# Kernel tuning notes

Measured on AMD Instinct MI355X. Metric: run time of the kernel, lower is better.

Reference implementation:

```python
import jax, jax.numpy as jnp
import numpy as np

B, S, D, HEADS, E, HID = 4, 2048, 512, 8, 8, 1365  # HID = int(D*4*2/3) per Expert_alt
CF, THRESH, TOPN = 2.0, 0.2, 2                      # capacity_factor_eval, threshold_eval, top-2
BAL_COEF, Z_COEF = 0.01, 0.001


def setup_inputs():
    key = jax.random.key(0)
    ks = jax.random.split(key, 8)
    f32 = jnp.float32
    return {
        'x': jax.random.normal(ks[0], (B, S, D), f32),
        'Wqkv': jax.random.normal(ks[1], (3 * D, D), f32) * (D ** -0.5),
        'bqkv': jnp.zeros((3 * D,), f32),
        'Wo': jax.random.normal(ks[2], (D, D), f32) * (D ** -0.5),
        'bo': jnp.zeros((D,), f32),
        'Wg': jax.random.normal(ks[3], (D, E), f32) * (D ** -0.5),
        'ln_g': jnp.ones((E, D), f32),
        'ln_b': jnp.zeros((E, D), f32),
        'W1': jax.random.normal(ks[4], (E, D, HID), f32) * (D ** -0.5),
        'b1': jnp.zeros((E, HID), f32),
        'W2': jax.random.normal(ks[5], (E, HID, D), f32) * (HID ** -0.5),
        'b2': jnp.zeros((E, D), f32),
    }


def _moe(x, Wg, ln_g, ln_b, W1, b1, W2, b2):
    # top-2 gated MoE with capacity-factor dispatch, grouped expert FFN, combine
    Bq, Sq, Dq = x.shape
    Eq = Wg.shape[1]
    C = int(CF * Sq * TOPN / Eq)  # expert capacity per batch row
    logits = x @ Wg                              # [B,S,E]
    probs = jax.nn.softmax(logits, -1)
    gvals, gidx = jax.lax.top_k(probs, 2)        # [B,S,2]
    use2 = (gvals[..., 1] > THRESH).astype(x.dtype)
    # priority order: all top-1 assignments first, then top-2
    e_idx = jnp.concatenate([gidx[..., 0], gidx[..., 1]], axis=1)          # [B,2S]
    assigned = jnp.concatenate([jnp.ones((Bq, Sq), x.dtype), use2], axis=1)
    onehot = jax.nn.one_hot(e_idx, Eq, dtype=x.dtype) * assigned[..., None]
    pos = (jnp.cumsum(onehot, axis=1) * onehot).sum(-1) - 1.0              # slot within expert
    keep = ((assigned > 0) & (pos >= 0) & (pos < C)).astype(x.dtype)
    slot = jnp.where(keep > 0, pos, C).astype(jnp.int32)                   # overflow -> slot C (dropped)
    b_idx = jnp.broadcast_to(jnp.arange(Bq)[:, None], (Bq, 2 * Sq))
    x2 = jnp.concatenate([x, x], axis=1) * keep[..., None]
    disp = jnp.zeros((Bq, Eq, C + 1, Dq), x.dtype).at[b_idx, e_idx, slot].add(x2)
    # grouped expert FFN: LayerNorm -> Linear -> LeakyReLU -> Linear
    xe = disp[:, :, :C].transpose(1, 0, 2, 3).reshape(Eq, Bq * C, Dq)
    mu = xe.mean(-1, keepdims=True)
    var = xe.var(-1, keepdims=True)
    xn = (xe - mu) * jax.lax.rsqrt(var + 1e-5) * ln_g[:, None] + ln_b[:, None]
    h = jnp.einsum('etd,edh->eth', xn, W1) + b1[:, None]
    h = jnp.where(h > 0, h, 0.01 * h)  # LeakyReLU
    ye = jnp.einsum('eth,ehd->etd', h, W2) + b2[:, None]
    yb = ye.reshape(Eq, Bq, C, Dq).transpose(1, 0, 2, 3)                   # [B,E,C,D]
    yb = jnp.concatenate([yb, jnp.zeros((Bq, Eq, 1, Dq), x.dtype)], axis=2)
    y_tok = yb[b_idx, e_idx, slot]                                         # [B,2S,D]
    w = jnp.concatenate([gvals[..., 0], gvals[..., 1] * use2], axis=1) * keep
    out = (y_tok * w[..., None]).reshape(Bq, 2, Sq, Dq).sum(1)
    # aux losses
    top1 = jax.nn.one_hot(gidx[..., 0], Eq, dtype=x.dtype)
    density = top1.mean((0, 1))
    proxy = probs.mean((0, 1))
    balance = Eq * jnp.sum(density * proxy)
    zloss = jnp.mean(jax.nn.logsumexp(logits, -1) ** 2)
    total = BAL_COEF * balance + Z_COEF * zloss
    return out, total, balance, zloss


def reference(x, Wqkv, bqkv, Wo, bo, Wg, ln_g, ln_b, W1, b1, W2, b2):
    Bq, Sq, Dq = x.shape
    dh = Dq // HEADS
    qkv = x @ Wqkv.T + bqkv
    q, k, v = jnp.split(qkv, 3, -1)
    rs = lambda t: t.reshape(Bq, Sq, HEADS, dh).transpose(0, 2, 1, 3)
    q, k, v = rs(q), rs(k), rs(v)
    attn = jax.nn.softmax(jnp.einsum('bhqd,bhkd->bhqk', q, k) / np.float32(np.sqrt(dh)), -1)
    o = jnp.einsum('bhqk,bhkd->bhqd', attn, v).transpose(0, 2, 1, 3).reshape(Bq, Sq, Dq)
    o = o @ Wo.T + bo + x  # MHA + residual
    moe_out, total, bal, z = _moe(o, Wg, ln_g, ln_b, W1, b1, W2, b2)
    return moe_out + o, total, bal, z  # SparseMoEBlock residual; dropout is identity (eval)
```

## Files before the change

kernel.cpp:

```cpp
#include <hip/hip_runtime.h>
#include <hip/hip_bf16.h>
#include <math.h>

#define B_    4
#define S_    2048
#define D_    512
#define H_    8
#define DH_   64
#define E_    8
#define HID_  1365
#define HIDP_ 1408
#define CAP_  1024
#define TOK_  (B_*S_)
#define NASS_ (B_*2*S_)
#define RMAX_ (NASS_ + 8*128)

typedef __attribute__((ext_vector_type(8))) short bf16x8;
typedef __attribute__((ext_vector_type(4))) float f32x4;
typedef __hip_bfloat16 bf16;

#define MFMA16(a, b, c) __builtin_amdgcn_mfma_f32_16x16x32_bf16(a, b, c, 0, 0, 0)

__device__ __forceinline__ void gload16(const void* g, void* l) {
  __builtin_amdgcn_global_load_lds(
      (const __attribute__((address_space(1))) unsigned int*)g,
      (__attribute__((address_space(3))) unsigned int*)l, 16, 0, 0);
}

__device__ __forceinline__ unsigned bf16pk(float a, float b) {
  unsigned ua = __float_as_uint(a); ua = (ua + 0x7FFF + ((ua >> 16) & 1)) >> 16;
  unsigned ub = __float_as_uint(b); ub = (ub + 0x7FFF + ((ub >> 16) & 1)) >> 16;
  return ua | (ub << 16);
}

__device__ __forceinline__ unsigned short bf16rne(float x, float& back) {
  unsigned u = __float_as_uint(x);
  unsigned r = (u + 0x7FFF + ((u >> 16) & 1)) >> 16;
  back = __uint_as_float(r << 16);
  return (unsigned short)r;
}

__global__ __launch_bounds__(256) void cvt_bf16(const float* __restrict__ in,
                                                bf16* __restrict__ out, int n) {
  int i = (blockIdx.x * 256 + threadIdx.x) * 4;
  if (i < n) {
    float4 v = *(const float4*)(in + i);
    uint2 pk; pk.x = bf16pk(v.x, v.y); pk.y = bf16pk(v.z, v.w);
    *(uint2*)((unsigned short*)out + i) = pk;
  }
}

__global__ __launch_bounds__(256) void split3v(const float* __restrict__ in,
    unsigned short* __restrict__ ph, unsigned short* __restrict__ pm,
    unsigned short* __restrict__ pl, int n) {
  int i = (blockIdx.x * 256 + threadIdx.x) * 4;
  if (i >= n) return;
  float4 v = *(const float4*)(in + i);
  float a[4] = {v.x, v.y, v.z, v.w};
  ushort4 hh, mm, ll;
  unsigned short* hp = (unsigned short*)&hh;
  unsigned short* mp = (unsigned short*)&mm;
  unsigned short* lp = (unsigned short*)&ll;
#pragma unroll
  for (int j = 0; j < 4; j++) {
    float fh, fm, fl;
    hp[j] = bf16rne(a[j], fh);
    float r = a[j] - fh;
    mp[j] = bf16rne(r, fm);
    float r2 = r - fm;
    lp[j] = bf16rne(r2, fl);
  }
  *(ushort4*)(ph + i) = hh;
  *(ushort4*)(pm + i) = mm;
  *(ushort4*)(pl + i) = ll;
}

__global__ __launch_bounds__(256) void transpose_w1(const float* __restrict__ W1,
                                                    bf16* __restrict__ W1t) {
  __shared__ float t[32][33];
  int e = blockIdx.z;
  int n0 = blockIdx.x * 32, d0 = blockIdx.y * 32;
  int tx = threadIdx.x & 31, ty = threadIdx.x >> 5;
  const float* in = W1 + (size_t)e * D_ * HID_;
  bf16* out = W1t + (size_t)e * HIDP_ * D_;
#pragma unroll
  for (int j = 0; j < 4; j++) {
    int d = d0 + ty + j * 8, n = n0 + tx;
    t[ty + j * 8][tx] = (n < HID_) ? in[(size_t)d * HID_ + n] : 0.f;
  }
  __syncthreads();
#pragma unroll
  for (int j = 0; j < 4; j++) {
    int n = n0 + ty + j * 8, d = d0 + tx;
    out[(size_t)n * D_ + d] = __float2bfloat16(t[tx][ty + j * 8]);
  }
}

__global__ __launch_bounds__(256) void transpose_w2(const float* __restrict__ W2,
                                                    bf16* __restrict__ W2t) {
  __shared__ float t[32][33];
  int e = blockIdx.z;
  int n0 = blockIdx.x * 32, k0 = blockIdx.y * 32;
  int tx = threadIdx.x & 31, ty = threadIdx.x >> 5;
  const float* in = W2 + (size_t)e * HID_ * D_;
  bf16* out = W2t + (size_t)e * D_ * HIDP_;
#pragma unroll
  for (int j = 0; j < 4; j++) {
    int k = k0 + ty + j * 8;
    t[ty + j * 8][tx] = (k < HID_) ? in[(size_t)k * D_ + n0 + tx] : 0.f;
  }
  __syncthreads();
#pragma unroll
  for (int j = 0; j < 4; j++) {
    int n = n0 + ty + j * 8, k = k0 + tx;
    out[(size_t)n * HIDP_ + k] = __float2bfloat16(t[tx][ty + j * 8]);
  }
}

__global__ __launch_bounds__(256) void transpose_v(const bf16* __restrict__ vbuf,
                                                   bf16* __restrict__ vT) {
  __shared__ bf16 t[32][33];
  int bh = blockIdx.z;
  int b = bh >> 3, h = bh & 7;
  int s0 = blockIdx.x * 32, d0 = blockIdx.y * 32;
  int tx = threadIdx.x & 31, ty = threadIdx.x >> 5;
  const bf16* in = vbuf + (size_t)b * S_ * D_ + h * DH_;
#pragma unroll
  for (int j = 0; j < 4; j++)
    t[ty + j * 8][tx] = in[(size_t)(s0 + ty + j * 8) * D_ + d0 + tx];
  __syncthreads();
  bf16* out = vT + (size_t)bh * DH_ * S_;
#pragma unroll
  for (int j = 0; j < 4; j++)
    out[(size_t)(d0 + ty + j * 8) * S_ + s0 + tx] = t[tx][ty + j * 8];
}

__global__ __launch_bounds__(256) void transpose_u(const float* __restrict__ U32,
                                                   bf16* __restrict__ U2T) {
  __shared__ float t[64][132];
  int b = blockIdx.y;
  int s0 = blockIdx.x * 64;
  int tid = threadIdx.x;
#pragma unroll
  for (int p = 0; p < 8; p++) {
    int i = tid + p * 256;
    int tok = i >> 5, c4 = i & 31;
    float4 v = *(const float4*)(U32 + (size_t)(b * 2048 + s0 + tok) * 128 + c4 * 4);
    t[tok][c4 * 4 + 0] = v.x; t[tok][c4 * 4 + 1] = v.y;
    t[tok][c4 * 4 + 2] = v.z; t[tok][c4 * 4 + 3] = v.w;
  }
  __syncthreads();
  int row = tid >> 1, sh = tid & 1;
  int h = row >> 4, rr = row & 15;
  int e = rr & 7;
  bool lo = rr >= 8;
  bf16* dst = U2T + ((size_t)((b * 8 + h) * 16 + rr) * 2048 + s0 + sh * 32);
  for (int i = 0; i < 32; i++) {
    float v = t[sh * 32 + i][h * 8 + e];
    float back;
    unsigned short hh = bf16rne(v, back);
    unsigned short outv;
    if (lo) { float b2; outv = bf16rne(v - back, b2); }
    else outv = hh;
    ((unsigned short*)dst)[i] = outv;
  }
}

template <int MODE>
__global__ __launch_bounds__(256) void gemm_mfma(
    const bf16* __restrict__ A, const bf16* __restrict__ Bt,
    const float* __restrict__ bias, const float* __restrict__ resid,
    void* __restrict__ Cout, int N, int K,
    const int* __restrict__ ebase, const int* __restrict__ ecnt) {
  __shared__ bf16 Al[128 * 64];
  __shared__ bf16 Bl[128 * 64];
  int tid = threadIdx.x;
  int w = tid >> 6, lane = tid & 63;
  int lg = lane >> 4, li = lane & 15;
  int e = 0;
  size_t arow0;
  if constexpr (MODE >= 2) {
    e = blockIdx.z;
    int r0 = blockIdx.y * 128;
    if (r0 >= ecnt[e]) return;
    arow0 = (size_t)(ebase[e] + r0);
  } else {
    arow0 = (size_t)blockIdx.y * 128;
  }
  int n0 = blockIdx.x * 128;
  const bf16* Bexp = Bt + (size_t)e * N * K;

  int rowA[4], scA[4];
#pragma unroll
  for (int j = 0; j < 4; j++) {
    int o = w * 4096 + j * 1024 + lane * 16;
    rowA[j] = o >> 7;
    scA[j] = ((o >> 4) & 7) ^ (rowA[j] & 7);
  }
  int wm = w >> 1, wn = w & 1;
  f32x4 acc[4][4] = {};

  for (int k0 = 0; k0 < K; k0 += 64) {
#pragma unroll
    for (int j = 0; j < 4; j++) {
      int o = w * 4096 + j * 1024 + lane * 16;
      gload16(A + (arow0 + rowA[j]) * (size_t)K + k0 + scA[j] * 8, (char*)Al + o);
      gload16(Bexp + (size_t)(n0 + rowA[j]) * K + k0 + scA[j] * 8, (char*)Bl + o);
    }
    __syncthreads();
#pragma unroll
    for (int ks = 0; ks < 2; ks++) {
      bf16x8 af[4], bfr[4];
#pragma unroll
      for (int mi = 0; mi < 4; mi++) {
        int row = wm * 64 + mi * 16 + li;
        int cb = (lg * 16 + ks * 64) ^ ((row & 7) << 4);
        af[mi] = *(const bf16x8*)((char*)Al + row * 128 + cb);
      }
#pragma unroll
      for (int ni = 0; ni < 4; ni++) {
        int row = wn * 64 + ni * 16 + li;
        int cb = (lg * 16 + ks * 64) ^ ((row & 7) << 4);
        bfr[ni] = *(const bf16x8*)((char*)Bl + row * 128 + cb);
      }
#pragma unroll
      for (int mi = 0; mi < 4; mi++)
#pragma unroll
        for (int ni = 0; ni < 4; ni++)
          acc[mi][ni] = MFMA16(af[mi], bfr[ni], acc[mi][ni]);
    }
    __syncthreads();
  }

#pragma unroll
  for (int mi = 0; mi < 4; mi++) {
#pragma unroll
    for (int ni = 0; ni < 4; ni++) {
#pragma unroll
      for (int r = 0; r < 4; r++) {
        size_t m = arow0 + wm * 64 + mi * 16 + lg * 4 + r;
        int c = n0 + wn * 64 + ni * 16 + li;
        float v = acc[mi][ni][r];
        if constexpr (MODE == 0) {
          v += bias[c];
          ((bf16*)Cout)[m * (size_t)N + c] = __float2bfloat16(v);
        } else if constexpr (MODE == 1) {
          v += bias[c] + resid[m * (size_t)N + c];
          ((float*)Cout)[m * (size_t)N + c] = v;
        } else if constexpr (MODE == 2) {
          if (c < HID_) {
            v += bias[e * HID_ + c];
            v = (v > 0.f) ? v : 0.01f * v;
            ((bf16*)Cout)[m * (size_t)HIDP_ + c] = __float2bfloat16(v);
          } else {
            ((bf16*)Cout)[m * (size_t)HIDP_ + c] = __float2bfloat16(0.f);
          }
        } else {
          v += bias[e * D_ + c];
          ((bf16*)Cout)[m * (size_t)N + c] = __float2bfloat16(v);
        }
      }
    }
  }
}

__global__ __launch_bounds__(256) void gemm_split3(
    const bf16* __restrict__ Ah, const bf16* __restrict__ Am, const bf16* __restrict__ Al_,
    const bf16* __restrict__ Bh, const bf16* __restrict__ Bm, const bf16* __restrict__ Bl_,
    const float* __restrict__ bias, float* __restrict__ C, int N, int K) {
  __shared__ bf16 Ls[6][128 * 32];
  const bf16* Ap[3] = {Ah, Am, Al_};
  const bf16* Bp[3] = {Bh, Bm, Bl_};
  int tid = threadIdx.x;
  int w = tid >> 6, lane = tid & 63;
  int lg = lane >> 4, li = lane & 15;
  int lin = blockIdx.y * gridDim.x + blockIdx.x;
  int lxn = (gridDim.x == 8) ? 3 : 0;
  int ytile = (lin & 7) + ((lin >> (3 + lxn)) << 3);
  int xtile = (lin >> 3) & (gridDim.x - 1);
  size_t m0 = (size_t)ytile * 128;
  int n0 = xtile * 128;
  int wm = w >> 1, wn = w & 1;
  f32x4 acc[4][4] = {};

  for (int k0 = 0; k0 < K; k0 += 32) {
#pragma unroll
    for (int p = 0; p < 3; p++) {
#pragma unroll
      for (int j = 0; j < 2; j++) {
        int o = w * 2048 + j * 1024 + lane * 16;
        int row = o >> 6;
        int sc = ((o >> 4) & 3) ^ (row & 3);
        gload16(Ap[p] + (m0 + row) * (size_t)K + k0 + sc * 8, (char*)Ls[p] + o);
        gload16(Bp[p] + (size_t)(n0 + row) * K + k0 + sc * 8, (char*)Ls[3 + p] + o);
      }
    }
    __syncthreads();
    bf16x8 af[3][4], bfv[3][4];
#pragma unroll
    for (int p = 0; p < 3; p++) {
#pragma unroll
      for (int mi = 0; mi < 4; mi++) {
        int row = wm * 64 + mi * 16 + li;
        int cb = (lg * 16) ^ ((row & 3) << 4);
        af[p][mi] = *(const bf16x8*)((char*)Ls[p] + row * 64 + cb);
      }
#pragma unroll
      for (int ni = 0; ni < 4; ni++) {
        int row = wn * 64 + ni * 16 + li;
        int cb = (lg * 16) ^ ((row & 3) << 4);
        bfv[p][ni] = *(const bf16x8*)((char*)Ls[3 + p] + row * 64 + cb);
      }
    }
#pragma unroll
    for (int mi = 0; mi < 4; mi++)
#pragma unroll
      for (int ni = 0; ni < 4; ni++) {
        acc[mi][ni] = MFMA16(af[0][mi], bfv[0][ni], acc[mi][ni]);
        acc[mi][ni] = MFMA16(af[0][mi], bfv[1][ni], acc[mi][ni]);
        acc[mi][ni] = MFMA16(af[1][mi], bfv[0][ni], acc[mi][ni]);
        acc[mi][ni] = MFMA16(af[1][mi], bfv[1][ni], acc[mi][ni]);
        acc[mi][ni] = MFMA16(af[0][mi], bfv[2][ni], acc[mi][ni]);
        acc[mi][ni] = MFMA16(af[2][mi], bfv[0][ni], acc[mi][ni]);
      }
    __syncthreads();
  }
#pragma unroll
  for (int mi = 0; mi < 4; mi++)
#pragma unroll
    for (int ni = 0; ni < 4; ni++)
#pragma unroll
      for (int r = 0; r < 4; r++) {
        size_t m = m0 + wm * 64 + mi * 16 + lg * 4 + r;
        int c = n0 + wn * 64 + ni * 16 + li;
        C[m * (size_t)N + c] = acc[mi][ni][r] + bias[c];
      }
}

__global__ __launch_bounds__(256) void ksplit(const float* __restrict__ qk32,
    unsigned short* __restrict__ kh, unsigned short* __restrict__ km,
    unsigned short* __restrict__ kl) {
  int gid = blockIdx.x * 256 + threadIdx.x;
  int idx4 = gid * 4;
  int t = idx4 >> 9, c = idx4 & 511;
  int h = c >> 6, d = c & 63;
  int b = t >> 11, s = t & 2047;
  float4 v = *(const float4*)(qk32 + (size_t)t * 1024 + 512 + c);
  float a[4] = {v.x, v.y, v.z, v.w};
  ushort4 hh, mm, ll;
  unsigned short* hp = (unsigned short*)&hh;
  unsigned short* mp = (unsigned short*)&mm;
  unsigned short* lp = (unsigned short*)&ll;
#pragma unroll
  for (int j = 0; j < 4; j++) {
    float fh, fm, fl;
    hp[j] = bf16rne(a[j], fh);
    float r = a[j] - fh;
    mp[j] = bf16rne(r, fm);
    float r2 = r - fm;
    lp[j] = bf16rne(r2, fl);
  }
  size_t o = (((size_t)(b * 8 + h) * S_ + s) * 64 + d);
  *(ushort4*)(kh + o) = hh;
  *(ushort4*)(km + o) = mm;
  *(ushort4*)(kl + o) = ll;
}

__global__ __launch_bounds__(256) void wg2_kernel(const float* __restrict__ Wo,
                                                  const float* __restrict__ Wg,
                                                  float* __restrict__ Wg2) {
  int gid = blockIdx.x * 256 + threadIdx.x;
  int d = gid >> 3, e = gid & 7;
  float acc = 0.f;
  for (int n = 0; n < D_; n++) acc += Wo[(size_t)n * D_ + d] * Wg[n * E_ + e];
  Wg2[d * E_ + e] = acc;
}

__global__ __launch_bounds__(256) void wu_kernel(const float* __restrict__ Wqkv,
    const float* __restrict__ Wg2, const float* __restrict__ bqkv,
    float* __restrict__ Wu, float* __restrict__ bU) {
  int gid = blockIdx.x * 256 + threadIdx.x;
  int row = gid >> 9, d = gid & 511;
  float acc = 0.f;
  if (row < 64) {
    int h = row >> 3, e = row & 7;
    const float* wv = Wqkv + (size_t)(1024 + h * 64) * 512 + d;
    const float* wg = Wg2 + h * 64 * 8 + e;
    for (int c = 0; c < 64; c++) acc += wv[(size_t)c * 512] * wg[c * 8];
  }
  Wu[gid] = acc;
  if (gid < 128) {
    float bacc = 0.f;
    if (gid < 64) {
      int h = gid >> 3, e = gid & 7;
      for (int c = 0; c < 64; c++)
        bacc += bqkv[1024 + h * 64 + c] * Wg2[(h * 64 + c) * 8 + e];
    }
    bU[gid] = bacc;
  }
}

__global__ __launch_bounds__(256) void xwg_kernel(const float* __restrict__ x,
                                                  const float* __restrict__ bo,
                                                  const float* __restrict__ Wg,
                                                  float* __restrict__ logits) {
  int tid = threadIdx.x;
  int tl = tid >> 3, j = tid & 7;
  int t = blockIdx.x * 32 + tl;
  const float* xr = x + (size_t)t * D_;
  float part[8] = {0, 0, 0, 0, 0, 0, 0, 0};
  for (int d = j; d < D_; d += 8) {
    float xv = xr[d] + bo[d];
    const float* wg = Wg + d * E_;
#pragma unroll
    for (int e = 0; e < 8; e++) part[e] += xv * wg[e];
  }
#pragma unroll
  for (int off = 1; off < 8; off <<= 1)
#pragma unroll
    for (int e = 0; e < 8; e++) part[e] += __shfl_xor(part[e], off);
  if (j == 0) {
#pragma unroll
    for (int e = 0; e < 8; e++) logits[(size_t)t * 8 + e] = part[e];
  }
}

__global__ __launch_bounds__(512, 4) void attn_fused(
    const float* __restrict__ qk32,
    const bf16* __restrict__ kh, const bf16* __restrict__ km,
    const bf16* __restrict__ kl,
    const bf16* __restrict__ vT, const bf16* __restrict__ U2T,
    bf16* __restrict__ attnb, float* __restrict__ part) {
  __shared__ bf16 Ks0[128 * 64];
  __shared__ bf16 Ks1[128 * 64];
  __shared__ bf16 Ks2[128 * 64];
  __shared__ bf16 Vtl[64 * 128];
  __shared__ bf16 Ut[16 * 128];
  __shared__ bf16 Pl[8][16 * 40];
  int bid = blockIdx.x;
  int xcd = bid & 7, idx = bid >> 3;
  int bh = (idx >> 4) * 8 + xcd;
  int qt = idx & 15;
  int b = bh >> 3, h = bh & 7, q0 = qt * 128;
  int tid = threadIdx.x, w = tid >> 6, lane = tid & 63;
  int lg = lane >> 4, qi = lane & 15;

  const float* qsrc = qk32 + (size_t)(b * S_ + q0 + w * 16 + qi) * 1024 + h * 64 + lg * 8;
  bf16x8 qh[2], qm[2], ql[2];
#pragma unroll
  for (int ks = 0; ks < 2; ks++) {
#pragma unroll
    for (int i = 0; i < 8; i++) {
      float xv = qsrc[ks * 32 + i];
      float fh, fm, fl;
      unsigned short ah = bf16rne(xv, fh);
      float r = xv - fh;
      unsigned short am = bf16rne(r, fm);
      float r2 = r - fm;
      unsigned short al = bf16rne(r2, fl);
      ((unsigned short*)&qh[ks])[i] = ah;
      ((unsigned short*)&qm[ks])[i] = am;
      ((unsigned short*)&ql[ks])[i] = al;
    }
  }

  f32x4 oacc[4] = {};
  f32x4 racc = {0.f, 0.f, 0.f, 0.f};
  float mrun = -1e30f, lrun = 0.f;
  const bf16* Vbase = vT + (size_t)bh * DH_ * S_;
  char* pw = (char*)&Pl[w][0];

  for (int kt = 0; kt < S_ / 128; kt++) {
#pragma unroll
    for (int j = 0; j < 2; j++) {
      int o = w * 2048 + j * 1024 + lane * 16;
      int row = o >> 7;
      int sc = ((o >> 4) & 7) ^ (row & 7);
      size_t srcK = ((size_t)bh * S_ + kt * 128 + row) * 64 + sc * 8;
      gload16(kh + srcK, (char*)Ks0 + o);
      gload16(km + srcK, (char*)Ks1 + o);
      gload16(kl + srcK, (char*)Ks2 + o);
      int rowv = o >> 8;
      int scv = ((o >> 4) & 15) ^ (rowv & 7);
      gload16(Vbase + (size_t)rowv * S_ + kt * 128 + scv * 8, (char*)Vtl + o);
    }
    if (w < 2) {
#pragma unroll
      for (int j = 0; j < 2; j++) {
        int o = w * 2048 + j * 1024 + lane * 16;
        int rowu = o >> 8;
        int scu = ((o >> 4) & 15) ^ (rowu & 7);
        gload16(U2T + ((size_t)(bh * 16 + rowu) * 2048 + kt * 128 + scu * 8),
                (char*)Ut + o);
      }
    }
    __syncthreads();

    f32x4 sacc[8];
#pragma unroll
    for (int nb = 0; nb < 8; nb++) { f32x4 z = {0.f, 0.f, 0.f, 0.f}; sacc[nb] = z; }
#pragma unroll
    for (int ks = 0; ks < 2; ks++) {
#pragma unroll
      for (int nb = 0; nb < 8; nb++) {
        int row = nb * 16 + qi;
        int cb = (lg * 16 + ks * 64) ^ ((row & 7) << 4);
        bf16x8 k0 = *(const bf16x8*)((char*)Ks0 + row * 128 + cb);
        bf16x8 k1 = *(const bf16x8*)((char*)Ks1 + row * 128 + cb);
        bf16x8 k2 = *(const bf16x8*)((char*)Ks2 + row * 128 + cb);
        sacc[nb] = MFMA16(k0, qh[ks], sacc[nb]);
        sacc[nb] = MFMA16(k0, qm[ks], sacc[nb]);
        sacc[nb] = MFMA16(k1, qh[ks], sacc[nb]);
        sacc[nb] = MFMA16(k1, qm[ks], sacc[nb]);
        sacc[nb] = MFMA16(k2, qh[ks], sacc[nb]);
        sacc[nb] = MFMA16(k0, ql[ks], sacc[nb]);
      }
    }
    float tmax = -1e30f;
#pragma unroll
    for (int nb = 0; nb < 8; nb++)
#pragma unroll
      for (int r = 0; r < 4; r++) {
        float v = sacc[nb][r] * 0.125f;
        sacc[nb][r] = v;
        tmax = fmaxf(tmax, v);
      }
    tmax = fmaxf(tmax, __shfl_xor(tmax, 16));
    tmax = fmaxf(tmax, __shfl_xor(tmax, 32));
    float mnew = fmaxf(mrun, tmax);
    float fsc = __expf(mrun - mnew);
    float psum = 0.f;
#pragma unroll
    for (int nb = 0; nb < 8; nb++)
#pragma unroll
      for (int r = 0; r < 4; r++) {
        float pv = __expf(sacc[nb][r] - mnew);
        sacc[nb][r] = pv;
        psum += pv;
      }
    psum += __shfl_xor(psum, 16);
    psum += __shfl_xor(psum, 32);
    lrun = lrun * fsc + psum;
    mrun = mnew;
#pragma unroll
    for (int r = 0; r < 4; r++) racc[r] *= fsc;
#pragma unroll
    for (int db = 0; db < 4; db++)
#pragma unroll
      for (int r = 0; r < 4; r++) oacc[db][r] *= fsc;

#pragma unroll
    for (int c = 0; c < 4; c++) {
#pragma unroll
      for (int nbL = 0; nbL < 2; nbL++) {
        int nb = c * 2 + nbL;
#pragma unroll
        for (int rp = 0; rp < 2; rp++) {
          unsigned pk = bf16pk(sacc[nb][rp * 2], sacc[nb][rp * 2 + 1]);
          int keyl = 4 * lg + 2 * rp + 16 * nbL;
          *(unsigned*)(pw + qi * 80 + keyl * 2) = pk;
        }
      }
      bf16x8 pf = *(const bf16x8*)(pw + qi * 80 + lg * 16);
#pragma unroll
      for (int db = 0; db < 4; db++) {
        int row = db * 16 + qi;
        int cb = (lg * 16 + c * 64) ^ ((row & 7) << 4);
        bf16x8 vf = *(const bf16x8*)((char*)Vtl + row * 256 + cb);
        oacc[db] = MFMA16(vf, pf, oacc[db]);
      }
      int ua = qi * 256 + ((c * 64 + lg * 16) ^ ((qi & 7) << 4));
      bf16x8 uf = *(const bf16x8*)((char*)Ut + ua);
      racc = MFMA16(uf, pf, racc);
#pragma unroll
      for (int nbL = 0; nbL < 2; nbL++) {
        int nb = c * 2 + nbL;
#pragma unroll
        for (int rp = 0; rp < 2; rp++) {
          float p0 = sacc[nb][rp * 2], p1 = sacc[nb][rp * 2 + 1];
          float b0, b1v;
          bf16rne(p0, b0); bf16rne(p1, b1v);
          unsigned pkl = bf16pk(p0 - b0, p1 - b1v);
          int keyl = 4 * lg + 2 * rp + 16 * nbL;
          *(unsigned*)(pw + qi * 80 + keyl * 2) = pkl;
        }
      }
      bf16x8 pfl = *(const bf16x8*)(pw + qi * 80 + lg * 16);
      racc = MFMA16(uf, pfl, racc);
    }
    __syncthreads();
  }

  float inv = 1.f / lrun;
#pragma unroll
  for (int r = 0; r < 4; r++) racc[r] += __shfl_xor(racc[r], 32);
  if (lg < 2) {
    float* dst = part + ((size_t)bh * S_ + q0 + w * 16 + qi) * 8 + lg * 4;
#pragma unroll
    for (int r = 0; r < 4; r++) dst[r] = racc[r] * inv;
  }
  char* ow = (char*)Ks0 + w * 2048;
#pragma unroll
  for (int db = 0; db < 4; db++)
#pragma unroll
    for (int rp = 0; rp < 2; rp++) {
      int d = db * 16 + lg * 4 + rp * 2;
      unsigned pk = bf16pk(oacc[db][rp * 2] * inv, oacc[db][rp * 2 + 1] * inv);
      int addr = (qi * 128 + d * 2) ^ ((qi & 7) << 4);
      *(unsigned*)(ow + addr) = pk;
    }
#pragma unroll
  for (int j = 0; j < 2; j++) {
    int o = j * 1024 + lane * 16;
    int q = o >> 7;
    int c16 = (o >> 4) & 7;
    int sc = c16 ^ (q & 7);
    bf16x8 vv = *(const bf16x8*)(ow + q * 128 + sc * 16);
    *(bf16x8*)(attnb + ((size_t)(b * S_ + q0 + w * 16 + q)) * D_ + h * DH_ + c16 * 8) = vv;
  }
}

__global__ __launch_bounds__(256) void reduce_gate(
    const float* __restrict__ xwg, const float* __restrict__ part,
    int* __restrict__ e1a, int* __restrict__ e2a,
    float* __restrict__ g1a, float* __restrict__ g2a, int* __restrict__ use2a,
    float* __restrict__ dacc) {
  int t = blockIdx.x * 256 + threadIdx.x;
  int b = t >> 11, s = t & 2047;
  float lg[8];
#pragma unroll
  for (int e = 0; e < 8; e++) lg[e] = xwg[(size_t)t * 8 + e];
  for (int h = 0; h < 8; h++) {
    const float* pp = part + ((size_t)(b * 8 + h) * S_ + s) * 8;
#pragma unroll
    for (int e = 0; e < 8; e++) lg[e] += pp[e];
  }
  float mx = lg[0];
#pragma unroll
  for (int e = 1; e < 8; e++) mx = fmaxf(mx, lg[e]);
  float p[8], se = 0.f;
#pragma unroll
  for (int e = 0; e < 8; e++) { p[e] = expf(lg[e] - mx); se += p[e]; }
  float inv = 1.f / se;
#pragma unroll
  for (int e = 0; e < 8; e++) p[e] *= inv;
  float lse = logf(se) + mx;
  int a1 = 0; float m1 = p[0];
#pragma unroll
  for (int e = 1; e < 8; e++) if (p[e] > m1) { m1 = p[e]; a1 = e; }
  int a2 = -1; float m2 = -1.f;
#pragma unroll
  for (int e = 0; e < 8; e++) if (e != a1 && p[e] > m2) { m2 = p[e]; a2 = e; }
  e1a[t] = a1; e2a[t] = a2; g1a[t] = m1; g2a[t] = m2;
  use2a[t] = (m2 > 0.2f) ? 1 : 0;
  float z = lse * lse;
  float pr[8];
#pragma unroll
  for (int e = 0; e < 8; e++) pr[e] = p[e];
#pragma unroll
  for (int off = 1; off < 64; off <<= 1) {
#pragma unroll
    for (int e = 0; e < 8; e++) pr[e] += __shfl_xor(pr[e], off);
    z += __shfl_xor(z, off);
  }
  float dcnt[8];
#pragma unroll
  for (int e = 0; e < 8; e++) dcnt[e] = (float)__popcll(__ballot(a1 == e));
  if ((threadIdx.x & 63) == 0) {
#pragma unroll
    for (int e = 0; e < 8; e++) {
      atomicAdd(&dacc[e], dcnt[e]);
      atomicAdd(&dacc[8 + e], pr[e]);
    }
    atomicAdd(&dacc[16], z);
  }
}

__global__ __launch_bounds__(512) void scan_kernel(
    const int* __restrict__ e1a, const int* __restrict__ e2a,
    const int* __restrict__ use2a,
    int* __restrict__ posArr, int* __restrict__ kept_be) {
  __shared__ int wcnt[8][8];
  int b = blockIdx.x;
  int w = threadIdx.x >> 6, lane = threadIdx.x & 63;
  unsigned long long below = (1ull << lane) - 1ull;
  int cnt[8] = {0, 0, 0, 0, 0, 0, 0, 0};
  int ev[8], av[8];
#pragma unroll
  for (int it = 0; it < 8; it++) {
    int i = w * 512 + it * 64 + lane;
    int s = i & (S_ - 1);
    int t = b * S_ + s;
    int e, a;
    if (i < S_) { e = e1a[t]; a = 1; }
    else        { e = e2a[t]; a = use2a[t]; }
    ev[it] = e; av[it] = a;
#pragma unroll
    for (int ee = 0; ee < 8; ee++)
      cnt[ee] += __popcll(__ballot(a && (e == ee)));
  }
  if (lane == 0)
#pragma unroll
    for (int ee = 0; ee < 8; ee++) wcnt[w][ee] = cnt[ee];
  __syncthreads();
  int run[8];
#pragma unroll
  for (int ee = 0; ee < 8; ee++) {
    int sB = 0;
    for (int ww = 0; ww < w; ww++) sB += wcnt[ww][ee];
    run[ee] = sB;
  }
#pragma unroll
  for (int it = 0; it < 8; it++) {
    int i = w * 512 + it * 64 + lane;
    int e = ev[it], a = av[it];
    int pos = -1;
#pragma unroll
    for (int ee = 0; ee < 8; ee++) {
      unsigned long long mask = __ballot(a && (e == ee));
      if (a && e == ee) pos = run[ee] + __popcll(mask & below);
      run[ee] += __popcll(mask);
    }
    posArr[b * (2 * S_) + i] = (a && pos < CAP_) ? pos : -1;
  }
  if (w == 7 && lane == 0)
#pragma unroll
    for (int ee = 0; ee < 8; ee++) kept_be[b * 8 + ee] = min(run[ee], CAP_);
}

__global__ void finalize_meta(const int* __restrict__ kept_be,
                              int* __restrict__ ebase, int* __restrict__ bbase,
                              int* __restrict__ ecnt,
                              const float* __restrict__ dacc, float* __restrict__ outs) {
  if (threadIdx.x == 0 && blockIdx.x == 0) {
    int base = 0;
    for (int e = 0; e < 8; e++) {
      int tot = 0;
      for (int b = 0; b < 4; b++) { bbase[b * 8 + e] = tot; tot += kept_be[b * 8 + e]; }
      ecnt[e] = tot;
      ebase[e] = base;
      base += (tot + 127) & ~127;
    }
    float bal = 0.f;
    for (int e = 0; e < 8; e++) bal += (dacc[e] / (float)TOK_) * (dacc[8 + e] / (float)TOK_);
    bal *= (float)E_;
    float z = dacc[16] / (float)TOK_;
    outs[0] = 0.01f * bal + 0.001f * z;
    outs[1] = bal;
    outs[2] = z;
  }
}

__global__ __launch_bounds__(256) void scatter_kernel(
    const int* __restrict__ posArr, const int* __restrict__ e1a, const int* __restrict__ e2a,
    const float* __restrict__ g1a, const float* __restrict__ g2a,
    const int* __restrict__ ebase, const int* __restrict__ bbase,
    int* __restrict__ rowtok, int* __restrict__ rowexp,
    int* __restrict__ tokidx, float* __restrict__ tokw) {
  int gi = blockIdx.x * 256 + threadIdx.x;
  int b = gi >> 12, i = gi & 4095;
  int k = i >> 11, s = i & (S_ - 1);
  int t = b * S_ + s;
  int pos = posArr[gi];
  int idx = -1; float w = 0.f;
  if (pos >= 0) {
    int e = k ? e2a[t] : e1a[t];
    idx = ebase[e] + bbase[b * 8 + e] + pos;
    rowtok[idx] = t;
    rowexp[idx] = e;
    w = k ? g2a[t] : g1a[t];
  }
  tokidx[k * TOK_ + t] = idx;
  tokw[k * TOK_ + t] = w;
}

__global__ __launch_bounds__(256) void ln_kernel(
    const float* __restrict__ o2, const int* __restrict__ rowtok,
    const int* __restrict__ rowexp, const float* __restrict__ ln_g,
    const float* __restrict__ ln_b, bf16* __restrict__ xn) {
  int row = blockIdx.x * 4 + (threadIdx.x >> 6);
  int lane = threadIdx.x & 63;
  int tok = rowtok[row];
  if (tok < 0) return;
  int e = rowexp[row];
  const float* xr = o2 + (size_t)tok * D_;
  float v[8], sum = 0.f, sq = 0.f;
#pragma unroll
  for (int j = 0; j < 8; j++) { v[j] = xr[lane * 8 + j]; sum += v[j]; sq += v[j] * v[j]; }
#pragma unroll
  for (int off = 1; off < 64; off <<= 1) { sum += __shfl_xor(sum, off); sq += __shfl_xor(sq, off); }
  float mu = sum / (float)D_;
  float var = sq / (float)D_ - mu * mu;
  float inv = rsqrtf(var + 1e-5f);
  bf16* xo = xn + (size_t)row * D_;
#pragma unroll
  for (int j = 0; j < 8; j++) {
    int d = lane * 8 + j;
    xo[d] = __float2bfloat16((v[j] - mu) * inv * ln_g[e * D_ + d] + ln_b[e * D_ + d]);
  }
}

__global__ __launch_bounds__(256) void combine_kernel(
    const float* __restrict__ o2, const bf16* __restrict__ y,
    const int* __restrict__ tokidx, const float* __restrict__ tokw,
    float* __restrict__ out) {
  size_t gi = (size_t)blockIdx.x * 256 + threadIdx.x;
  int t = (int)(gi >> 9);
  int d = (int)(gi & (D_ - 1));
  float v = o2[gi];
  int i1 = tokidx[t], i2 = tokidx[TOK_ + t];
  if (i1 >= 0) v += tokw[t] * __bfloat162float(y[(size_t)i1 * D_ + d]);
  if (i2 >= 0) v += tokw[TOK_ + t] * __bfloat162float(y[(size_t)i2 * D_ + d]);
  out[gi] = v;
}

extern "C" void kernel_launch(void* const* d_in, const int* in_sizes, int n_in,
                              void* d_out, int out_size, void* d_ws, size_t ws_size,
                              hipStream_t stream) {
  const float* x    = (const float*)d_in[0];
  const float* Wqkv = (const float*)d_in[1];
  const float* bqkv = (const float*)d_in[2];
  const float* Wo   = (const float*)d_in[3];
  const float* bo   = (const float*)d_in[4];
  const float* Wg   = (const float*)d_in[5];
  const float* ln_g = (const float*)d_in[6];
  const float* ln_b = (const float*)d_in[7];
  const float* W1   = (const float*)d_in[8];
  const float* b1   = (const float*)d_in[9];
  const float* W2   = (const float*)d_in[10];
  const float* b2   = (const float*)d_in[11];
  float* out = (float*)d_out;

  char* ws = (char*)d_ws;
  size_t off = 0;
  auto alloc = [&](size_t bytes) -> void* {
    void* p = ws + off;
    off = (off + bytes + 255) & ~(size_t)255;
    return p;
  };
  float* qk32  = (float*)alloc((size_t)TOK_ * 1024 * 4);
  bf16* vbuf   = (bf16*)alloc((size_t)TOK_ * D_ * 2);
  bf16* vT     = (bf16*)alloc((size_t)B_ * H_ * DH_ * S_ * 2);
  bf16* attnb  = (bf16*)alloc((size_t)TOK_ * D_ * 2);
  float* o2    = (float*)alloc((size_t)TOK_ * D_ * 4);
  bf16* xh     = (bf16*)alloc((size_t)TOK_ * D_ * 2);
  bf16* xm     = (bf16*)alloc((size_t)TOK_ * D_ * 2);
  bf16* xl     = (bf16*)alloc((size_t)TOK_ * D_ * 2);
  bf16* Wqh    = (bf16*)alloc((size_t)1024 * D_ * 2);
  bf16* Wqm    = (bf16*)alloc((size_t)1024 * D_ * 2);
  bf16* Wql    = (bf16*)alloc((size_t)1024 * D_ * 2);
  bf16* Wvb    = (bf16*)alloc((size_t)D_ * D_ * 2);
  bf16* Wob    = (bf16*)alloc((size_t)D_ * D_ * 2);
  bf16* W1t    = (bf16*)alloc((size_t)E_ * HIDP_ * D_ * 2);
  bf16* W2t    = (bf16*)alloc((size_t)E_ * D_ * HIDP_ * 2);
  bf16* xn     = (bf16*)alloc((size_t)RMAX_ * D_ * 2);
  bf16* hbuf   = (bf16*)alloc((size_t)RMAX_ * HIDP_ * 2);
  bf16* ybuf   = (bf16*)alloc((size_t)RMAX_ * D_ * 2);
  float* Wg2   = (float*)alloc(D_ * E_ * 4);
  float* Wu    = (float*)alloc((size_t)128 * D_ * 4);
  float* bU    = (float*)alloc(128 * 4);
  bf16* Wuh    = (bf16*)alloc((size_t)128 * D_ * 2);
  bf16* Wum    = (bf16*)alloc((size_t)128 * D_ * 2);
  bf16* Wul    = (bf16*)alloc((size_t)128 * D_ * 2);
  float* U32   = (float*)alloc((size_t)TOK_ * 128 * 4);
  bf16* U2T    = (bf16*)alloc((size_t)32 * 16 * 2048 * 2);
  float* logits= (float*)alloc((size_t)TOK_ * 8 * 4);
  float* part  = (float*)alloc((size_t)B_ * H_ * S_ * 8 * 4);
  int*   e1a   = (int*)alloc(TOK_ * 4);
  int*   e2a   = (int*)alloc(TOK_ * 4);
  int*   use2a = (int*)alloc(TOK_ * 4);
  float* g1a   = (float*)alloc(TOK_ * 4);
  float* g2a   = (float*)alloc(TOK_ * 4);
  int*   posArr  = (int*)alloc(NASS_ * 4);
  int*   kept_be = (int*)alloc(32 * 4);
  int*   ebase   = (int*)alloc(8 * 4);
  int*   bbase   = (int*)alloc(32 * 4);
  int*   ecnt    = (int*)alloc(8 * 4);
  int*   rowtok  = (int*)alloc(RMAX_ * 4);
  int*   rowexp  = (int*)alloc(RMAX_ * 4);
  int*   tokidx  = (int*)alloc(NASS_ * 4);
  float* tokw    = (float*)alloc(NASS_ * 4);
  float* dacc    = (float*)alloc(32 * 4);
  bf16* kh = xh;
  bf16* km = xm;
  bf16* kl = xl;

  hipMemsetAsync(dacc, 0, 32 * 4, stream);
  hipMemsetAsync(rowtok, 0xFF, RMAX_ * 4, stream);

  split3v<<<TOK_ * D_ / 4 / 256, 256, 0, stream>>>(x, (unsigned short*)xh,
                                                   (unsigned short*)xm,
                                                   (unsigned short*)xl, TOK_ * D_);
  split3v<<<1024 * D_ / 4 / 256, 256, 0, stream>>>(Wqkv, (unsigned short*)Wqh,
                                                   (unsigned short*)Wqm,
                                                   (unsigned short*)Wql, 1024 * D_);
  cvt_bf16<<<D_ * D_ / 4 / 256, 256, 0, stream>>>(Wqkv + (size_t)1024 * D_, Wvb, D_ * D_);
  cvt_bf16<<<D_ * D_ / 4 / 256, 256, 0, stream>>>(Wo, Wob, D_ * D_);
  transpose_w1<<<dim3(44, 16, 8), 256, 0, stream>>>(W1, W1t);
  transpose_w2<<<dim3(16, 44, 8), 256, 0, stream>>>(W2, W2t);
  wg2_kernel<<<16, 256, 0, stream>>>(Wo, Wg, Wg2);
  wu_kernel<<<256, 256, 0, stream>>>(Wqkv, Wg2, bqkv, Wu, bU);
  split3v<<<128 * D_ / 4 / 256, 256, 0, stream>>>(Wu, (unsigned short*)Wuh,
                                                  (unsigned short*)Wum,
                                                  (unsigned short*)Wul, 128 * D_);

  gemm_split3<<<dim3(8, 64), 256, 0, stream>>>(xh, xm, xl, Wqh, Wqm, Wql,
                                               bqkv, qk32, 1024, D_);
  gemm_split3<<<dim3(1, 64), 256, 0, stream>>>(xh, xm, xl, Wuh, Wum, Wul,
                                               bU, U32, 128, D_);
  gemm_mfma<0><<<dim3(4, 64), 256, 0, stream>>>(xh, Wvb, bqkv + 1024, nullptr, vbuf,
                                                D_, D_, nullptr, nullptr);
  ksplit<<<TOK_ * 512 / 4 / 256, 256, 0, stream>>>(qk32, (unsigned short*)kh,
                                                   (unsigned short*)km,
                                                   (unsigned short*)kl);
  transpose_u<<<dim3(32, 4), 256, 0, stream>>>(U32, U2T);
  xwg_kernel<<<TOK_ / 32, 256, 0, stream>>>(x, bo, Wg, logits);
  transpose_v<<<dim3(64, 2, 32), 256, 0, stream>>>(vbuf, vT);

  attn_fused<<<dim3(512), 512, 0, stream>>>(qk32, kh, km, kl, vT, U2T,
                                            attnb, part);
  gemm_mfma<1><<<dim3(4, 64), 256, 0, stream>>>(attnb, Wob, bo, x, o2,
                                                D_, D_, nullptr, nullptr);
  reduce_gate<<<TOK_ / 256, 256, 0, stream>>>(logits, part, e1a, e2a, g1a, g2a,
                                              use2a, dacc);
  scan_kernel<<<B_, 512, 0, stream>>>(e1a, e2a, use2a, posArr, kept_be);
  finalize_meta<<<1, 64, 0, stream>>>(kept_be, ebase, bbase, ecnt, dacc,
                                      out + (size_t)TOK_ * D_);
  scatter_kernel<<<NASS_ / 256, 256, 0, stream>>>(posArr, e1a, e2a, g1a, g2a,
                                                  ebase, bbase, rowtok, rowexp,
                                                  tokidx, tokw);
  ln_kernel<<<RMAX_ / 4, 256, 0, stream>>>(o2, rowtok, rowexp, ln_g, ln_b, xn);
  gemm_mfma<2><<<dim3(HIDP_ / 128, 32, E_), 256, 0, stream>>>(xn, W1t, b1, nullptr, hbuf,
                                                              HIDP_, D_, ebase, ecnt);
  gemm_mfma<3><<<dim3(D_ / 128, 32, E_), 256, 0, stream>>>(hbuf, W2t, b2, nullptr, ybuf,
                                                           D_, HIDP_, ebase, ecnt);
  combine_kernel<<<(TOK_ * D_) / 256, 256, 0, stream>>>(o2, ybuf, tokidx, tokw, out);
}
```

Baseline: 533.1 us.

## Fuse U projection into QK split3 GEMM and hoist P hi/lo splitting

The separate 128-column U projection GEMM is merged into the QK split-precision GEMM by appending the Wu rows to the Wq weight buffers, giving one 1152-wide output buffer and a combined bias. This removes a kernel launch and a separate pass over the x split operands. The grouped tile swizzle in gemm_split3 is dropped because the grid width is now 9. In attention, the bf16 hi/lo split of P is computed once up front instead of recomputing the rounding inside the low pass, which costs extra registers.

```diff
diff --git a/kernel.cpp b/kernel.cpp
--- a/kernel.cpp
+++ b/kernel.cpp
@@ -14,6 +14,7 @@
 #define TOK_  (B_*S_)
 #define NASS_ (B_*2*S_)
 #define RMAX_ (NASS_ + 8*128)
+#define NQKU_ 1152
 
 typedef __attribute__((ext_vector_type(8))) short bf16x8;
 typedef __attribute__((ext_vector_type(4))) float f32x4;
@@ -135,7 +136,7 @@
     out[(size_t)(d0 + ty + j * 8) * S_ + s0 + tx] = t[tx][ty + j * 8];
 }
 
-__global__ __launch_bounds__(256) void transpose_u(const float* __restrict__ U32,
+__global__ __launch_bounds__(256) void transpose_u(const float* __restrict__ qku,
                                                    bf16* __restrict__ U2T) {
   __shared__ float t[64][132];
   int b = blockIdx.y;
@@ -145,7 +146,7 @@
   for (int p = 0; p < 8; p++) {
     int i = tid + p * 256;
     int tok = i >> 5, c4 = i & 31;
-    float4 v = *(const float4*)(U32 + (size_t)(b * 2048 + s0 + tok) * 128 + c4 * 4);
+    float4 v = *(const float4*)(qku + (size_t)(b * 2048 + s0 + tok) * NQKU_ + 1024 + c4 * 4);
     t[tok][c4 * 4 + 0] = v.x; t[tok][c4 * 4 + 1] = v.y;
     t[tok][c4 * 4 + 2] = v.z; t[tok][c4 * 4 + 3] = v.w;
   }
@@ -274,12 +275,8 @@
   int tid = threadIdx.x;
   int w = tid >> 6, lane = tid & 63;
   int lg = lane >> 4, li = lane & 15;
-  int lin = blockIdx.y * gridDim.x + blockIdx.x;
-  int lxn = (gridDim.x == 8) ? 3 : 0;
-  int ytile = (lin & 7) + ((lin >> (3 + lxn)) << 3);
-  int xtile = (lin >> 3) & (gridDim.x - 1);
-  size_t m0 = (size_t)ytile * 128;
-  int n0 = xtile * 128;
+  size_t m0 = (size_t)blockIdx.y * 128;
+  int n0 = blockIdx.x * 128;
   int wm = w >> 1, wn = w & 1;
   f32x4 acc[4][4] = {};
 
@@ -337,7 +334,7 @@
       }
 }
 
-__global__ __launch_bounds__(256) void ksplit(const float* __restrict__ qk32,
+__global__ __launch_bounds__(256) void ksplit(const float* __restrict__ qku,
     unsigned short* __restrict__ kh, unsigned short* __restrict__ km,
     unsigned short* __restrict__ kl) {
   int gid = blockIdx.x * 256 + threadIdx.x;
@@ -345,7 +342,7 @@
   int t = idx4 >> 9, c = idx4 & 511;
   int h = c >> 6, d = c & 63;
   int b = t >> 11, s = t & 2047;
-  float4 v = *(const float4*)(qk32 + (size_t)t * 1024 + 512 + c);
+  float4 v = *(const float4*)(qku + (size_t)t * NQKU_ + 512 + c);
   float a[4] = {v.x, v.y, v.z, v.w};
   ushort4 hh, mm, ll;
   unsigned short* hp = (unsigned short*)&hh;
@@ -378,7 +375,7 @@
 
 __global__ __launch_bounds__(256) void wu_kernel(const float* __restrict__ Wqkv,
     const float* __restrict__ Wg2, const float* __restrict__ bqkv,
-    float* __restrict__ Wu, float* __restrict__ bU) {
+    float* __restrict__ Wu, float* __restrict__ bfull) {
   int gid = blockIdx.x * 256 + threadIdx.x;
   int row = gid >> 9, d = gid & 511;
   float acc = 0.f;
@@ -389,6 +386,7 @@
     for (int c = 0; c < 64; c++) acc += wv[(size_t)c * 512] * wg[c * 8];
   }
   Wu[gid] = acc;
+  if (gid < 1024) bfull[gid] = bqkv[gid];
   if (gid < 128) {
     float bacc = 0.f;
     if (gid < 64) {
@@ -396,7 +394,7 @@
       for (int c = 0; c < 64; c++)
         bacc += bqkv[1024 + h * 64 + c] * Wg2[(h * 64 + c) * 8 + e];
     }
-    bU[gid] = bacc;
+    bfull[1024 + gid] = bacc;
   }
 }
 
@@ -426,7 +424,7 @@
 }
 
 __global__ __launch_bounds__(512, 4) void attn_fused(
-    const float* __restrict__ qk32,
+    const float* __restrict__ qku,
     const bf16* __restrict__ kh, const bf16* __restrict__ km,
     const bf16* __restrict__ kl,
     const bf16* __restrict__ vT, const bf16* __restrict__ U2T,
@@ -445,7 +443,7 @@
   int tid = threadIdx.x, w = tid >> 6, lane = tid & 63;
   int lg = lane >> 4, qi = lane & 15;
 
-  const float* qsrc = qk32 + (size_t)(b * S_ + q0 + w * 16 + qi) * 1024 + h * 64 + lg * 8;
+  const float* qsrc = qku + (size_t)(b * S_ + q0 + w * 16 + qi) * NQKU_ + h * 64 + lg * 8;
   bf16x8 qh[2], qm[2], ql[2];
 #pragma unroll
   for (int ks = 0; ks < 2; ks++) {
@@ -549,18 +547,30 @@
 #pragma unroll
       for (int r = 0; r < 4; r++) oacc[db][r] *= fsc;
 
+    unsigned hw[16], lw[16];
+#pragma unroll
+    for (int nb = 0; nb < 8; nb++)
+#pragma unroll
+      for (int rp = 0; rp < 2; rp++) {
+        float p0 = sacc[nb][rp * 2], p1 = sacc[nb][rp * 2 + 1];
+        unsigned u0 = __float_as_uint(p0), u1 = __float_as_uint(p1);
+        unsigned h0 = (u0 + 0x7FFF + ((u0 >> 16) & 1)) >> 16;
+        unsigned h1 = (u1 + 0x7FFF + ((u1 >> 16) & 1)) >> 16;
+        hw[nb * 2 + rp] = h0 | (h1 << 16);
+        float r0 = p0 - __uint_as_float(h0 << 16);
+        float r1 = p1 - __uint_as_float(h1 << 16);
+        lw[nb * 2 + rp] = bf16pk(r0, r1);
+      }
+
 #pragma unroll
     for (int c = 0; c < 4; c++) {
 #pragma unroll
-      for (int nbL = 0; nbL < 2; nbL++) {
-        int nb = c * 2 + nbL;
+      for (int nbL = 0; nbL < 2; nbL++)
 #pragma unroll
         for (int rp = 0; rp < 2; rp++) {
-          unsigned pk = bf16pk(sacc[nb][rp * 2], sacc[nb][rp * 2 + 1]);
           int keyl = 4 * lg + 2 * rp + 16 * nbL;
-          *(unsigned*)(pw + qi * 80 + keyl * 2) = pk;
+          *(unsigned*)(pw + qi * 80 + keyl * 2) = hw[(c * 2 + nbL) * 2 + rp];
         }
-      }
       bf16x8 pf = *(const bf16x8*)(pw + qi * 80 + lg * 16);
 #pragma unroll
       for (int db = 0; db < 4; db++) {
@@ -573,18 +583,12 @@
       bf16x8 uf = *(const bf16x8*)((char*)Ut + ua);
       racc = MFMA16(uf, pf, racc);
 #pragma unroll
-      for (int nbL = 0; nbL < 2; nbL++) {
-        int nb = c * 2 + nbL;
+      for (int nbL = 0; nbL < 2; nbL++)
 #pragma unroll
         for (int rp = 0; rp < 2; rp++) {
-          float p0 = sacc[nb][rp * 2], p1 = sacc[nb][rp * 2 + 1];
-          float b0, b1v;
-          bf16rne(p0, b0); bf16rne(p1, b1v);
-          unsigned pkl = bf16pk(p0 - b0, p1 - b1v);
           int keyl = 4 * lg + 2 * rp + 16 * nbL;
-          *(unsigned*)(pw + qi * 80 + keyl * 2) = pkl;
+          *(unsigned*)(pw + qi * 80 + keyl * 2) = lw[(c * 2 + nbL) * 2 + rp];
         }
-      }
       bf16x8 pfl = *(const bf16x8*)(pw + qi * 80 + lg * 16);
       racc = MFMA16(uf, pfl, racc);
     }
@@ -838,7 +842,7 @@
     off = (off + bytes + 255) & ~(size_t)255;
     return p;
   };
-  float* qk32  = (float*)alloc((size_t)TOK_ * 1024 * 4);
+  float* qku32 = (float*)alloc((size_t)TOK_ * NQKU_ * 4);
   bf16* vbuf   = (bf16*)alloc((size_t)TOK_ * D_ * 2);
   bf16* vT     = (bf16*)alloc((size_t)B_ * H_ * DH_ * S_ * 2);
   bf16* attnb  = (bf16*)alloc((size_t)TOK_ * D_ * 2);
@@ -846,9 +850,9 @@
   bf16* xh     = (bf16*)alloc((size_t)TOK_ * D_ * 2);
   bf16* xm     = (bf16*)alloc((size_t)TOK_ * D_ * 2);
   bf16* xl     = (bf16*)alloc((size_t)TOK_ * D_ * 2);
-  bf16* Wqh    = (bf16*)alloc((size_t)1024 * D_ * 2);
-  bf16* Wqm    = (bf16*)alloc((size_t)1024 * D_ * 2);
-  bf16* Wql    = (bf16*)alloc((size_t)1024 * D_ * 2);
+  bf16* Wqh    = (bf16*)alloc((size_t)NQKU_ * D_ * 2);
+  bf16* Wqm    = (bf16*)alloc((size_t)NQKU_ * D_ * 2);
+  bf16* Wql    = (bf16*)alloc((size_t)NQKU_ * D_ * 2);
   bf16* Wvb    = (bf16*)alloc((size_t)D_ * D_ * 2);
   bf16* Wob    = (bf16*)alloc((size_t)D_ * D_ * 2);
   bf16* W1t    = (bf16*)alloc((size_t)E_ * HIDP_ * D_ * 2);
@@ -858,11 +862,7 @@
   bf16* ybuf   = (bf16*)alloc((size_t)RMAX_ * D_ * 2);
   float* Wg2   = (float*)alloc(D_ * E_ * 4);
   float* Wu    = (float*)alloc((size_t)128 * D_ * 4);
-  float* bU    = (float*)alloc(128 * 4);
-  bf16* Wuh    = (bf16*)alloc((size_t)128 * D_ * 2);
-  bf16* Wum    = (bf16*)alloc((size_t)128 * D_ * 2);
-  bf16* Wul    = (bf16*)alloc((size_t)128 * D_ * 2);
-  float* U32   = (float*)alloc((size_t)TOK_ * 128 * 4);
+  float* bfull = (float*)alloc(NQKU_ * 4);
   bf16* U2T    = (bf16*)alloc((size_t)32 * 16 * 2048 * 2);
   float* logits= (float*)alloc((size_t)TOK_ * 8 * 4);
   float* part  = (float*)alloc((size_t)B_ * H_ * S_ * 8 * 4);
@@ -899,25 +899,24 @@
   transpose_w1<<<dim3(44, 16, 8), 256, 0, stream>>>(W1, W1t);
   transpose_w2<<<dim3(16, 44, 8), 256, 0, stream>>>(W2, W2t);
   wg2_kernel<<<16, 256, 0, stream>>>(Wo, Wg, Wg2);
-  wu_kernel<<<256, 256, 0, stream>>>(Wqkv, Wg2, bqkv, Wu, bU);
-  split3v<<<128 * D_ / 4 / 256, 256, 0, stream>>>(Wu, (unsigned short*)Wuh,
-                                                  (unsigned short*)Wum,
-                                                  (unsigned short*)Wul, 128 * D_);
-
-  gemm_split3<<<dim3(8, 64), 256, 0, stream>>>(xh, xm, xl, Wqh, Wqm, Wql,
-                                               bqkv, qk32, 1024, D_);
-  gemm_split3<<<dim3(1, 64), 256, 0, stream>>>(xh, xm, xl, Wuh, Wum, Wul,
-                                               bU, U32, 128, D_);
+  wu_kernel<<<256, 256, 0, stream>>>(Wqkv, Wg2, bqkv, Wu, bfull);
+  split3v<<<128 * D_ / 4 / 256, 256, 0, stream>>>(Wu,
+      (unsigned short*)(Wqh + (size_t)1024 * D_),
+      (unsigned short*)(Wqm + (size_t)1024 * D_),
+      (unsigned short*)(Wql + (size_t)1024 * D_), 128 * D_);
+
+  gemm_split3<<<dim3(9, 64), 256, 0, stream>>>(xh, xm, xl, Wqh, Wqm, Wql,
+                                               bfull, qku32, NQKU_, D_);
   gemm_mfma<0><<<dim3(4, 64), 256, 0, stream>>>(xh, Wvb, bqkv + 1024, nullptr, vbuf,
                                                 D_, D_, nullptr, nullptr);
-  ksplit<<<TOK_ * 512 / 4 / 256, 256, 0, stream>>>(qk32, (unsigned short*)kh,
+  ksplit<<<TOK_ * 512 / 4 / 256, 256, 0, stream>>>(qku32, (unsigned short*)kh,
                                                    (unsigned short*)km,
                                                    (unsigned short*)kl);
-  transpose_u<<<dim3(32, 4), 256, 0, stream>>>(U32, U2T);
+  transpose_u<<<dim3(32, 4), 256, 0, stream>>>(qku32, U2T);
   xwg_kernel<<<TOK_ / 32, 256, 0, stream>>>(x, bo, Wg, logits);
   transpose_v<<<dim3(64, 2, 32), 256, 0, stream>>>(vbuf, vT);
 
-  attn_fused<<<dim3(512), 512, 0, stream>>>(qk32, kh, km, kl, vT, U2T,
+  attn_fused<<<dim3(512), 512, 0, stream>>>(qku32, kh, km, kl, vT, U2T,
                                             attnb, part);
   gemm_mfma<1><<<dim3(4, 64), 256, 0, stream>>>(attnb, Wob, bo, x, o2,
                                                 D_, D_, nullptr, nullptr);
```

Result: slower. 545.4 us (+2.3%).
